# Performance work log

Hardware: AMD Instinct MI355X
Metric: run time of the kernel (lower is better)

## Reference

```python
import jax, jax.numpy as jnp
import numpy as np


def _conv3d(x, w, pad, groups=1):
    # x: [N,C,D,H,W]; w: [O,I/groups,kd,kh,kw]; cross-correlation, same as torch conv3d
    return jax.lax.conv_general_dilated(
        x, w, window_strides=(1, 1, 1),
        padding=[(p, p) for p in pad],
        dimension_numbers=('NCDHW', 'OIDHW', 'NCDHW'),
        feature_group_count=groups)


def setup_inputs() -> dict:
    key = jax.random.key(0)
    D = 192
    x = jax.random.normal(key, (1, 1, D, D, D), dtype=jnp.float32)

    # Gaussian kernel: sigma=1.0 -> radius=3 -> 7^3
    sigma = 1.0
    radius = int(3 * sigma)
    c = jnp.arange(-radius, radius + 1, dtype=jnp.float32)
    g1 = jnp.exp(-c ** 2 / (2.0 * sigma * sigma))
    g1 = g1 / g1.sum()
    g3 = g1[:, None, None] * g1[None, :, None] * g1[None, None, :]
    gauss3d = g3[None, None]  # [1,1,7,7,7]

    # Pavel derivative kernels (outer products of d [len 9] and s [len 5])
    d = jnp.array([2.0, 1.0, -16.0, -27.0, 0.0, 27.0, 16.0, -1.0, -2.0], dtype=jnp.float32)
    s = jnp.array([1.0, 4.0, 6.0, 4.0, 1.0], dtype=jnp.float32)
    norm = 96.0 * 16.0 * 16.0
    kz = (d[:, None, None] * s[None, :, None] * s[None, None, :] / norm)[None, None]  # [1,1,9,5,5]
    ky = (s[:, None, None] * d[None, :, None] * s[None, None, :] / norm)[None, None]  # [1,1,5,9,5]
    kx = (s[:, None, None] * s[None, :, None] * d[None, None, :] / norm)[None, None]  # [1,1,5,5,9]

    return {"x": x, "gauss3d": gauss3d, "kz": kz, "ky": ky, "kx": kx}


def reference(x, gauss3d, kz, ky, kx):
    pad = (gauss3d.shape[2] - 1) // 2  # radius = 3
    # sigma > 0: pre-smooth input
    xs = _conv3d(x, gauss3d, (pad, pad, pad))
    # gradient components
    gz = _conv3d(xs, kz, (4, 2, 2))
    gy = _conv3d(xs, ky, (2, 4, 2))
    gx = _conv3d(xs, kx, (2, 2, 4))
    # structure-tensor components, channel order [Jzz, Jzy, Jzx, Jyy, Jyx, Jxx]
    J = jnp.concatenate([gz * gz, gy * gz, gx * gz, gy * gy, gx * gy, gx * gx], axis=1)
    # smooth_components=True: grouped Gaussian smoothing of each component
    g6 = jnp.broadcast_to(gauss3d, (6,) + gauss3d.shape[1:])  # [6,1,7,7,7]
    J = _conv3d(J, g6, (pad, pad, pad), groups=6)
    return J
```

## Files before the change

### kernel.cpp

```cpp
#include <hip/hip_runtime.h>


constexpr int D  = 192;
constexpr int DD = D * D;
constexpr long long V = (long long)D * DD;

__global__ void setup_coef(const float* __restrict__ g3, const float* __restrict__ kz,
                           const float* __restrict__ ky, const float* __restrict__ kx,
                           float* __restrict__ c) {
    if (blockIdx.x != 0 || threadIdx.x != 0) return;
    float Tg = g3[0];
    for (int i = 0; i < 7; ++i) c[0 + i]  = g3[i * 49];
    for (int j = 0; j < 7; ++j) c[7 + j]  = g3[j * 7] / Tg;
    for (int k = 0; k < 7; ++k) c[14 + k] = g3[k] / Tg;
    float Tz = kz[0];
    for (int i = 0; i < 9; ++i) c[21 + i] = kz[i * 25];
    for (int j = 0; j < 5; ++j) c[30 + j] = kz[j * 5] / Tz;
    for (int k = 0; k < 5; ++k) c[35 + k] = kz[k] / Tz;
    float Ty = ky[0];
    for (int i = 0; i < 5; ++i) c[40 + i] = ky[i * 45];
    for (int j = 0; j < 9; ++j) c[45 + j] = ky[j * 5] / Ty;
    for (int k = 0; k < 5; ++k) c[54 + k] = ky[k] / Ty;
    float Tx = kx[0];
    for (int i = 0; i < 5; ++i) c[59 + i] = kx[i * 45];
    for (int j = 0; j < 5; ++j) c[64 + j] = kx[j * 9] / Tx;
    for (int k = 0; k < 9; ++k) c[69 + k] = kx[k] / Tx;
}

__device__ inline float4 ldg4(const float* __restrict__ slice, int gy, int gx) {
    float4 v = {0.f, 0.f, 0.f, 0.f};
    if ((unsigned)gy < (unsigned)D) {
        const float* row = slice + gy * D;
        if ((unsigned)gx <= (unsigned)(D - 4)) {
            v = *(const float4*)(row + gx);
        } else {
            float* pv = (float*)&v;
#pragma unroll
            for (int j = 0; j < 4; ++j) {
                const int g = gx + j;
                if ((unsigned)g < (unsigned)D) pv[j] = row[g];
            }
        }
    }
    return v;
}

__device__ inline void ldg4x2(const float* __restrict__ slA, const float* __restrict__ slB,
                              int gy, int gx, float4& a, float4& b) {
    a = make_float4(0.f, 0.f, 0.f, 0.f);
    b = a;
    if ((unsigned)gy < (unsigned)D) {
        const int ro = gy * D;
        if ((unsigned)gx <= (unsigned)(D - 4)) {
            a = *(const float4*)(slA + ro + gx);
            b = *(const float4*)(slB + ro + gx);
        } else {
            float* pa = (float*)&a;
            float* pb = (float*)&b;
#pragma unroll
            for (int j = 0; j < 4; ++j) {
                const int g = gx + j;
                if ((unsigned)g < (unsigned)D) { pa[j] = slA[ro + g]; pb[j] = slB[ro + g]; }
            }
        }
    }
}

__device__ inline float4 ld_task10(const float* __restrict__ slice, int y0, int x0, int li) {
    const int r = li / 10, q = li % 10;
    return ldg4(slice, y0 + r, x0 + q * 4);
}
__device__ inline void st_task41(float* __restrict__ dst, int li, float4 v) {
    const int r = li / 10, q = li % 10;
    float* d = &dst[r * 41 + q * 4];
    d[0] = v.x; d[1] = v.y; d[2] = v.z; d[3] = v.w;
}

template <int SEG>
__global__ __launch_bounds__(256) void blur3d_s1(const float* __restrict__ in,
                                                 float* __restrict__ out,
                                                 const float* __restrict__ coef) {
    __shared__ float raw[22 * 41];
    __shared__ float xt[22][32];
    const int cpx = gridDim.x >> 3;
    int w = (blockIdx.x & 7) * cpx + (blockIdx.x >> 3);
    const int tile = w % 72;
    const int seg = w / 72;
    const int tx0 = (tile % 6) * 32, ty0 = (tile / 6) * 16;
    const int z0 = seg * SEG;
    float ga[7], gb[7], gc[7];
#pragma unroll
    for (int k = 0; k < 7; ++k) { ga[k] = coef[k]; gb[k] = coef[7 + k]; gc[k] = coef[14 + k]; }
    const int tid = threadIdx.x;
    const int rr = tid >> 4;
    const int cc = (tid & 15) * 2;
    float2 ring[7];
#pragma unroll
    for (int k = 0; k < 7; ++k) ring[k] = make_float2(0.f, 0.f);

    for (int s = z0 - 3; s < z0 + SEG + 3; ++s) {
        const bool inz = (s >= 0 && s < D);
        if (inz && tid < 220) {
            const float* sl = in + (long long)s * DD;
            st_task41(raw, tid, ld_task10(sl, ty0 - 3, tx0 - 4, tid));
        }
        __syncthreads();
        if (inz && tid < 176) {
            const int r = tid >> 3, g = tid & 7;
            const float* rp = &raw[r * 41 + 4 * g + 1];
            float win[10];
#pragma unroll
            for (int i = 0; i < 10; ++i) win[i] = rp[i];
            float4 o = make_float4(0.f, 0.f, 0.f, 0.f);
#pragma unroll
            for (int k = 0; k < 7; ++k) {
                o.x += gc[k] * win[k];
                o.y += gc[k] * win[k + 1];
                o.z += gc[k] * win[k + 2];
                o.w += gc[k] * win[k + 3];
            }
            *(float4*)&xt[r][4 * g] = o;
        }
        __syncthreads();
        float2 yv = make_float2(0.f, 0.f);
        if (inz) {
#pragma unroll
            for (int k = 0; k < 7; ++k) {
                const float2 v = *(const float2*)&xt[rr + k][cc];
                yv.x += gb[k] * v.x; yv.y += gb[k] * v.y;
            }
        }
#pragma unroll
        for (int k = 0; k < 6; ++k) ring[k] = ring[k + 1];
        ring[6] = yv;
        const int z = s - 3;
        if (z >= z0) {
            float2 a = make_float2(0.f, 0.f);
#pragma unroll
            for (int k = 0; k < 7; ++k) {
                a.x += ga[k] * ring[k].x; a.y += ga[k] * ring[k].y;
            }
            *(float2*)(out + (long long)z * DD + (ty0 + rr) * D + tx0 + cc) = a;
        }
    }
}

template <int SEG, int NCH, bool PROD>
__global__ __launch_bounds__(256) void blur3d(const float* __restrict__ in,
                                              float* __restrict__ out,
                                              const float* __restrict__ coef) {
    __shared__ float raw[38 * 41];
    __shared__ float xt[38][32];
    const int cpx = gridDim.x >> 3;
    int w = (blockIdx.x & 7) * cpx + (blockIdx.x >> 3);
    const int tile = w % 36; w /= 36;
    const int ch = w % NCH;
    const int seg = w / NCH;
    const int tx0 = (tile % 6) * 32, ty0 = (tile / 6) * 32;
    const int z0 = seg * SEG;
    const int IA[6] = {0, 1, 2, 1, 2, 2};
    const int IB[6] = {0, 0, 0, 1, 1, 2};
    const float* srcA = in + (long long)(PROD ? IA[ch] : ch) * V;
    const float* srcB = in + (long long)(PROD ? IB[ch] : ch) * V;
    const bool same = !PROD || (IA[ch] == IB[ch]);
    float* dst = out + (long long)ch * V;
    float ga[7], gb[7], gc[7];
#pragma unroll
    for (int k = 0; k < 7; ++k) { ga[k] = coef[k]; gb[k] = coef[7 + k]; gc[k] = coef[14 + k]; }
    const int rr = threadIdx.x >> 3;
    const int cc = (threadIdx.x & 7) * 4;
    float4 ring[7];
#pragma unroll
    for (int k = 0; k < 7; ++k) ring[k] = make_float4(0.f, 0.f, 0.f, 0.f);

    for (int s = z0 - 3; s < z0 + SEG + 3; ++s) {
        const bool inz = (s >= 0 && s < D);
        if (inz) {
            const float* slA = srcA + (long long)s * DD;
            const float* slB = srcB + (long long)s * DD;
            if (same) {
                for (int li = threadIdx.x; li < 380; li += 256) {
                    float4 a = ld_task10(slA, ty0 - 3, tx0 - 4, li);
                    if (PROD) { a.x *= a.x; a.y *= a.y; a.z *= a.z; a.w *= a.w; }
                    st_task41(raw, li, a);
                }
            } else {
                for (int li = threadIdx.x; li < 380; li += 256) {
                    const int r = li / 10, q = li % 10;
                    float4 a, b;
                    ldg4x2(slA, slB, ty0 - 3 + r, tx0 - 4 + q * 4, a, b);
                    a.x *= b.x; a.y *= b.y; a.z *= b.z; a.w *= b.w;
                    float* d = &raw[r * 41 + q * 4];
                    d[0] = a.x; d[1] = a.y; d[2] = a.z; d[3] = a.w;
                }
            }
        }
        __syncthreads();
        if (inz) {
            for (int li = threadIdx.x; li < 38 * 8; li += 256) {
                const int r = li >> 3, g = li & 7;
                const float* rp = &raw[r * 41 + 4 * g + 1];
                float win[10];
#pragma unroll
                for (int i = 0; i < 10; ++i) win[i] = rp[i];
                float4 o = make_float4(0.f, 0.f, 0.f, 0.f);
#pragma unroll
                for (int k = 0; k < 7; ++k) {
                    o.x += gc[k] * win[k];
                    o.y += gc[k] * win[k + 1];
                    o.z += gc[k] * win[k + 2];
                    o.w += gc[k] * win[k + 3];
                }
                *(float4*)&xt[r][4 * g] = o;
            }
        }
        __syncthreads();
        float4 yv = make_float4(0.f, 0.f, 0.f, 0.f);
        if (inz) {
#pragma unroll
            for (int k = 0; k < 7; ++k) {
                const float4 v = *(const float4*)&xt[rr + k][cc];
                yv.x += gb[k] * v.x; yv.y += gb[k] * v.y;
                yv.z += gb[k] * v.z; yv.w += gb[k] * v.w;
            }
        }
#pragma unroll
        for (int k = 0; k < 6; ++k) ring[k] = ring[k + 1];
        ring[6] = yv;
        const int z = s - 3;
        if (z >= z0) {
            float4 a = make_float4(0.f, 0.f, 0.f, 0.f);
#pragma unroll
            for (int k = 0; k < 7; ++k) {
                a.x += ga[k] * ring[k].x; a.y += ga[k] * ring[k].y;
                a.z += ga[k] * ring[k].z; a.w += ga[k] * ring[k].w;
            }
            *(float4*)(dst + (long long)z * DD + (ty0 + rr) * D + tx0 + cc) = a;
        }
    }
}

template <int SEG>
__global__ __launch_bounds__(256) void grad3d(const float* __restrict__ xs,
                                              float* __restrict__ G,
                                              const float* __restrict__ coef) {
    __shared__ float raw[24 * 41];
    __shared__ float X1[24][32];
    __shared__ float X2[24][32];
    const int cpx = gridDim.x >> 3;
    int w = (blockIdx.x & 7) * cpx + (blockIdx.x >> 3);
    const int tile = w % 72;
    const int seg = w / 72;
    const int tx0 = (tile % 6) * 32, ty0 = (tile / 6) * 16;
    const int z0 = seg * SEG;
    float az[9], ay[5], ax[5], bz[5], by[9], bx[5], czc[5], cxc[9];
#pragma unroll
    for (int k = 0; k < 9; ++k) az[k] = coef[21 + k];
#pragma unroll
    for (int k = 0; k < 5; ++k) ay[k] = coef[40 + k];
#pragma unroll
    for (int k = 0; k < 5; ++k) ax[k] = coef[59 + k];
#pragma unroll
    for (int k = 0; k < 5; ++k) bz[k] = coef[30 + k];
#pragma unroll
    for (int k = 0; k < 9; ++k) by[k] = coef[45 + k];
#pragma unroll
    for (int k = 0; k < 5; ++k) bx[k] = coef[64 + k];
#pragma unroll
    for (int k = 0; k < 5; ++k) czc[k] = coef[35 + k];
#pragma unroll
    for (int k = 0; k < 9; ++k) cxc[k] = coef[69 + k];
    const int rr = threadIdx.x >> 4;
    const int cc = (threadIdx.x & 15) * 2;
    float2 R1[9], R2[7], R3[7];
#pragma unroll
    for (int k = 0; k < 9; ++k) R1[k] = make_float2(0.f, 0.f);
#pragma unroll
    for (int k = 0; k < 7; ++k) { R2[k] = make_float2(0.f, 0.f); R3[k] = make_float2(0.f, 0.f); }

    for (int s = z0 - 4; s < z0 + SEG + 4; ++s) {
        const bool inz = (s >= 0 && s < D);
        if (inz) {
            const float* sl = xs + (long long)s * DD;
            for (int li = threadIdx.x; li < 240; li += 256)
                st_task41(raw, li, ld_task10(sl, ty0 - 4, tx0 - 4, li));
        }
        __syncthreads();
        if (inz && threadIdx.x < 192) {
            const int r = threadIdx.x >> 3, g = threadIdx.x & 7;
            const float* rp = &raw[r * 41 + 4 * g];
            float win[12];
#pragma unroll
            for (int i = 0; i < 12; ++i) win[i] = rp[i];
            float4 o1 = make_float4(0.f, 0.f, 0.f, 0.f);
            float4 o2 = make_float4(0.f, 0.f, 0.f, 0.f);
#pragma unroll
            for (int k = 0; k < 5; ++k) {
                o1.x += czc[k] * win[2 + k];
                o1.y += czc[k] * win[3 + k];
                o1.z += czc[k] * win[4 + k];
                o1.w += czc[k] * win[5 + k];
            }
#pragma unroll
            for (int k = 0; k < 9; ++k) {
                o2.x += cxc[k] * win[k];
                o2.y += cxc[k] * win[1 + k];
                o2.z += cxc[k] * win[2 + k];
                o2.w += cxc[k] * win[3 + k];
            }
            *(float4*)&X1[r][4 * g] = o1;
            *(float4*)&X2[r][4 * g] = o2;
        }
        __syncthreads();
        float2 t1 = make_float2(0.f, 0.f), t2 = t1, t3 = t1;
        if (inz) {
#pragma unroll
            for (int k = 0; k < 5; ++k) {
                const float2 v = *(const float2*)&X1[rr + 2 + k][cc];
                t1.x += bz[k] * v.x; t1.y += bz[k] * v.y;
            }
#pragma unroll
            for (int k = 0; k < 9; ++k) {
                const float2 v = *(const float2*)&X1[rr + k][cc];
                t2.x += by[k] * v.x; t2.y += by[k] * v.y;
            }
#pragma unroll
            for (int k = 0; k < 5; ++k) {
                const float2 v = *(const float2*)&X2[rr + 2 + k][cc];
                t3.x += bx[k] * v.x; t3.y += bx[k] * v.y;
            }
        }
#pragma unroll
        for (int k = 0; k < 8; ++k) R1[k] = R1[k + 1];
        R1[8] = t1;
#pragma unroll
        for (int k = 0; k < 6; ++k) { R2[k] = R2[k + 1]; R3[k] = R3[k + 1]; }
        R2[6] = t2; R3[6] = t3;
        const int z = s - 4;
        if (z >= z0) {
            float gz0 = 0.f, gz1 = 0.f, gy0 = 0.f, gy1 = 0.f, gx0 = 0.f, gx1 = 0.f;
#pragma unroll
            for (int k = 0; k < 9; ++k) { gz0 += az[k] * R1[k].x; gz1 += az[k] * R1[k].y; }
#pragma unroll
            for (int k = 0; k < 5; ++k) {
                gy0 += ay[k] * R2[k].x; gy1 += ay[k] * R2[k].y;
                gx0 += ax[k] * R3[k].x; gx1 += ax[k] * R3[k].y;
            }
            float* o = G + (long long)z * DD + (ty0 + rr) * D + tx0 + cc;
            float2 wv;
            wv.x = gz0; wv.y = gz1; *(float2*)(o + 0 * V) = wv;
            wv.x = gy0; wv.y = gy1; *(float2*)(o + 1 * V) = wv;
            wv.x = gx0; wv.y = gx1; *(float2*)(o + 2 * V) = wv;
        }
    }
}

extern "C" void kernel_launch(void* const* d_in, const int* in_sizes, int n_in,
                              void* d_out, int out_size, void* d_ws, size_t ws_size,
                              hipStream_t stream) {
    const float* x  = (const float*)d_in[0];
    const float* g3 = (const float*)d_in[1];
    const float* kz = (const float*)d_in[2];
    const float* ky = (const float*)d_in[3];
    const float* kx = (const float*)d_in[4];
    float* out = (float*)d_out;

    float* coef = (float*)d_ws;
    float* G  = coef + 128;
    float* xs = G + 3 * V;

    setup_coef<<<1, 64, 0, stream>>>(g3, kz, ky, kx, coef);

    blur3d_s1<12><<<1152, 256, 0, stream>>>(x, xs, coef);

    grad3d<16><<<864, 256, 0, stream>>>(xs, G, coef);

    blur3d<32, 6, true><<<1296, 256, 0, stream>>>(G, out, coef);
}
```

Before: 164.9 us.

## Group structure-tensor products into two blocks of three channels per tile

Replaces the per-channel product-and-blur kernel with a grouped kernel in which each block loads the gradient slices once and forms three products (Jzz,Jzy,Jzx or Jyy,Jyx,Jxx), blurring all three together. This cuts redundant global reads of the gradient fields, which were previously reloaded for every output channel. Tiles change to 32x16 with a z-segment of 24, so shared memory and register use go up (three ring buffers, three xt tiles), which may lower occupancy.

```diff
diff --git a/kernel.cpp b/kernel.cpp
--- a/kernel.cpp
+++ b/kernel.cpp
@@ -45,27 +45,6 @@
     return v;
 }
 
-__device__ inline void ldg4x2(const float* __restrict__ slA, const float* __restrict__ slB,
-                              int gy, int gx, float4& a, float4& b) {
-    a = make_float4(0.f, 0.f, 0.f, 0.f);
-    b = a;
-    if ((unsigned)gy < (unsigned)D) {
-        const int ro = gy * D;
-        if ((unsigned)gx <= (unsigned)(D - 4)) {
-            a = *(const float4*)(slA + ro + gx);
-            b = *(const float4*)(slB + ro + gx);
-        } else {
-            float* pa = (float*)&a;
-            float* pb = (float*)&b;
-#pragma unroll
-            for (int j = 0; j < 4; ++j) {
-                const int g = gx + j;
-                if ((unsigned)g < (unsigned)D) { pa[j] = slA[ro + g]; pb[j] = slB[ro + g]; }
-            }
-        }
-    }
-}
-
 __device__ inline float4 ld_task10(const float* __restrict__ slice, int y0, int x0, int li) {
     const int r = li / 10, q = li % 10;
     return ldg4(slice, y0 + r, x0 + q * 4);
@@ -145,97 +124,117 @@
     }
 }
 
-template <int SEG, int NCH, bool PROD>
-__global__ __launch_bounds__(256) void blur3d(const float* __restrict__ in,
-                                              float* __restrict__ out,
-                                              const float* __restrict__ coef) {
-    __shared__ float raw[38 * 41];
-    __shared__ float xt[38][32];
+template <int SEG>
+__global__ __launch_bounds__(256) void blur3d_grp(const float* __restrict__ G,
+                                                  float* __restrict__ out,
+                                                  const float* __restrict__ coef) {
+    __shared__ float raw[3][22 * 41];
+    __shared__ float xt[3][22][32];
     const int cpx = gridDim.x >> 3;
     int w = (blockIdx.x & 7) * cpx + (blockIdx.x >> 3);
-    const int tile = w % 36; w /= 36;
-    const int ch = w % NCH;
-    const int seg = w / NCH;
-    const int tx0 = (tile % 6) * 32, ty0 = (tile / 6) * 32;
+    const int tile = w % 72; w /= 72;
+    const int grp = w & 1;
+    const int seg = w >> 1;
+    const int tx0 = (tile % 6) * 32, ty0 = (tile / 6) * 16;
     const int z0 = seg * SEG;
-    const int IA[6] = {0, 1, 2, 1, 2, 2};
-    const int IB[6] = {0, 0, 0, 1, 1, 2};
-    const float* srcA = in + (long long)(PROD ? IA[ch] : ch) * V;
-    const float* srcB = in + (long long)(PROD ? IB[ch] : ch) * V;
-    const bool same = !PROD || (IA[ch] == IB[ch]);
-    float* dst = out + (long long)ch * V;
+    const int nf = grp ? 2 : 3;
+    const float* F0 = G + (long long)(grp ? 1 : 0) * V;
+    const float* F1 = G + (long long)(grp ? 2 : 1) * V;
+    const float* F2 = G + 2 * V;
+    float* dst = out + (long long)(grp * 3) * V;
     float ga[7], gb[7], gc[7];
 #pragma unroll
     for (int k = 0; k < 7; ++k) { ga[k] = coef[k]; gb[k] = coef[7 + k]; gc[k] = coef[14 + k]; }
-    const int rr = threadIdx.x >> 3;
-    const int cc = (threadIdx.x & 7) * 4;
-    float4 ring[7];
-#pragma unroll
-    for (int k = 0; k < 7; ++k) ring[k] = make_float4(0.f, 0.f, 0.f, 0.f);
+    const int tid = threadIdx.x;
+    const int rr = tid >> 4;
+    const int cc = (tid & 15) * 2;
+    float2 R0[7], R1[7], R2[7];
+#pragma unroll
+    for (int k = 0; k < 7; ++k) {
+        R0[k] = make_float2(0.f, 0.f);
+        R1[k] = make_float2(0.f, 0.f);
+        R2[k] = make_float2(0.f, 0.f);
+    }
 
     for (int s = z0 - 3; s < z0 + SEG + 3; ++s) {
         const bool inz = (s >= 0 && s < D);
         if (inz) {
-            const float* slA = srcA + (long long)s * DD;
-            const float* slB = srcB + (long long)s * DD;
-            if (same) {
-                for (int li = threadIdx.x; li < 380; li += 256) {
-                    float4 a = ld_task10(slA, ty0 - 3, tx0 - 4, li);
-                    if (PROD) { a.x *= a.x; a.y *= a.y; a.z *= a.z; a.w *= a.w; }
-                    st_task41(raw, li, a);
+            const long long so = (long long)s * DD;
+            for (int li = tid; li < nf * 220; li += 256) {
+                const int f = li / 220, t = li - f * 220;
+                const float* sl = (f == 0 ? F0 : (f == 1 ? F1 : F2)) + so;
+                st_task41(raw[f], t, ld_task10(sl, ty0 - 3, tx0 - 4, t));
+            }
+        }
+        __syncthreads();
+        if (inz && tid < 176) {
+            const int r = tid >> 3, g = tid & 7;
+            const int off = r * 41 + 4 * g + 1;
+            float wA[10], wB[10];
+#pragma unroll
+            for (int i = 0; i < 10; ++i) { wA[i] = raw[0][off + i]; wB[i] = raw[1][off + i]; }
+            float p0[10], p1[10], p2[10];
+            if (grp == 0) {
+                float wC[10];
+#pragma unroll
+                for (int i = 0; i < 10; ++i) wC[i] = raw[2][off + i];
+#pragma unroll
+                for (int i = 0; i < 10; ++i) {
+                    p0[i] = wA[i] * wA[i];
+                    p1[i] = wB[i] * wA[i];
+                    p2[i] = wC[i] * wA[i];
                 }
             } else {
-                for (int li = threadIdx.x; li < 380; li += 256) {
-                    const int r = li / 10, q = li % 10;
-                    float4 a, b;
-                    ldg4x2(slA, slB, ty0 - 3 + r, tx0 - 4 + q * 4, a, b);
-                    a.x *= b.x; a.y *= b.y; a.z *= b.z; a.w *= b.w;
-                    float* d = &raw[r * 41 + q * 4];
-                    d[0] = a.x; d[1] = a.y; d[2] = a.z; d[3] = a.w;
+#pragma unroll
+                for (int i = 0; i < 10; ++i) {
+                    p0[i] = wA[i] * wA[i];
+                    p1[i] = wB[i] * wA[i];
+                    p2[i] = wB[i] * wB[i];
                 }
             }
-        }
-        __syncthreads();
-        if (inz) {
-            for (int li = threadIdx.x; li < 38 * 8; li += 256) {
-                const int r = li >> 3, g = li & 7;
-                const float* rp = &raw[r * 41 + 4 * g + 1];
-                float win[10];
-#pragma unroll
-                for (int i = 0; i < 10; ++i) win[i] = rp[i];
-                float4 o = make_float4(0.f, 0.f, 0.f, 0.f);
-#pragma unroll
-                for (int k = 0; k < 7; ++k) {
-                    o.x += gc[k] * win[k];
-                    o.y += gc[k] * win[k + 1];
-                    o.z += gc[k] * win[k + 2];
-                    o.w += gc[k] * win[k + 3];
-                }
-                *(float4*)&xt[r][4 * g] = o;
-            }
-        }
-        __syncthreads();
-        float4 yv = make_float4(0.f, 0.f, 0.f, 0.f);
-        if (inz) {
-#pragma unroll
-            for (int k = 0; k < 7; ++k) {
-                const float4 v = *(const float4*)&xt[rr + k][cc];
-                yv.x += gb[k] * v.x; yv.y += gb[k] * v.y;
-                yv.z += gb[k] * v.z; yv.w += gb[k] * v.w;
-            }
-        }
-#pragma unroll
-        for (int k = 0; k < 6; ++k) ring[k] = ring[k + 1];
-        ring[6] = yv;
+            float4 o0 = make_float4(0.f, 0.f, 0.f, 0.f), o1 = o0, o2 = o0;
+#pragma unroll
+            for (int k = 0; k < 7; ++k) {
+                o0.x += gc[k] * p0[k];     o0.y += gc[k] * p0[k + 1];
+                o0.z += gc[k] * p0[k + 2]; o0.w += gc[k] * p0[k + 3];
+                o1.x += gc[k] * p1[k];     o1.y += gc[k] * p1[k + 1];
+                o1.z += gc[k] * p1[k + 2]; o1.w += gc[k] * p1[k + 3];
+                o2.x += gc[k] * p2[k];     o2.y += gc[k] * p2[k + 1];
+                o2.z += gc[k] * p2[k + 2]; o2.w += gc[k] * p2[k + 3];
+            }
+            *(float4*)&xt[0][r][4 * g] = o0;
+            *(float4*)&xt[1][r][4 * g] = o1;
+            *(float4*)&xt[2][r][4 * g] = o2;
+        }
+        __syncthreads();
+        float2 y0 = make_float2(0.f, 0.f), y1 = y0, y2 = y0;
+        if (inz) {
+#pragma unroll
+            for (int k = 0; k < 7; ++k) {
+                const float2 v0 = *(const float2*)&xt[0][rr + k][cc];
+                const float2 v1 = *(const float2*)&xt[1][rr + k][cc];
+                const float2 v2 = *(const float2*)&xt[2][rr + k][cc];
+                y0.x += gb[k] * v0.x; y0.y += gb[k] * v0.y;
+                y1.x += gb[k] * v1.x; y1.y += gb[k] * v1.y;
+                y2.x += gb[k] * v2.x; y2.y += gb[k] * v2.y;
+            }
+        }
+#pragma unroll
+        for (int k = 0; k < 6; ++k) { R0[k] = R0[k + 1]; R1[k] = R1[k + 1]; R2[k] = R2[k + 1]; }
+        R0[6] = y0; R1[6] = y1; R2[6] = y2;
         const int z = s - 3;
         if (z >= z0) {
-            float4 a = make_float4(0.f, 0.f, 0.f, 0.f);
-#pragma unroll
-            for (int k = 0; k < 7; ++k) {
-                a.x += ga[k] * ring[k].x; a.y += ga[k] * ring[k].y;
-                a.z += ga[k] * ring[k].z; a.w += ga[k] * ring[k].w;
-            }
-            *(float4*)(dst + (long long)z * DD + (ty0 + rr) * D + tx0 + cc) = a;
+            float2 a0 = make_float2(0.f, 0.f), a1 = a0, a2 = a0;
+#pragma unroll
+            for (int k = 0; k < 7; ++k) {
+                a0.x += ga[k] * R0[k].x; a0.y += ga[k] * R0[k].y;
+                a1.x += ga[k] * R1[k].x; a1.y += ga[k] * R1[k].y;
+                a2.x += ga[k] * R2[k].x; a2.y += ga[k] * R2[k].y;
+            }
+            float* o = dst + (long long)z * DD + (ty0 + rr) * D + tx0 + cc;
+            *(float2*)(o + 0 * V) = a0;
+            *(float2*)(o + 1 * V) = a1;
+            *(float2*)(o + 2 * V) = a2;
         }
     }
 }
@@ -375,5 +374,5 @@
 
     grad3d<16><<<864, 256, 0, stream>>>(xs, G, coef);
 
-    blur3d<32, 6, true><<<1296, 256, 0, stream>>>(G, out, coef);
-}
+    blur3d_grp<24><<<1152, 256, 0, stream>>>(G, out, coef);
+}
```

Measured after the change: 205.8 us. 24.8% more time.

## Double-buffer shared staging in final blur to overlap loads and drop a barrier

Applied to the files above, without the earlier changes.

The six-channel product blur kernel now keeps two shared raw/xt buffers. It prefetches the next z-slice's product tile while computing the current slice's x-pass, which removes one __syncthreads per slice. This is meant to hide global load latency behind compute and reduce barrier stalls. In exchange, shared memory per block doubles, which could lower occupancy.

```diff
diff --git a/kernel.cpp b/kernel.cpp
--- a/kernel.cpp
+++ b/kernel.cpp
@@ -76,6 +76,27 @@
     d[0] = v.x; d[1] = v.y; d[2] = v.z; d[3] = v.w;
 }
 
+template <bool PROD>
+__device__ inline void stage_s3(const float* __restrict__ slA, const float* __restrict__ slB,
+                                bool same, float* __restrict__ dst, int ty0, int tx0) {
+    if (same) {
+        for (int li = threadIdx.x; li < 380; li += 256) {
+            float4 a = ld_task10(slA, ty0 - 3, tx0 - 4, li);
+            if (PROD) { a.x *= a.x; a.y *= a.y; a.z *= a.z; a.w *= a.w; }
+            st_task41(dst, li, a);
+        }
+    } else {
+        for (int li = threadIdx.x; li < 380; li += 256) {
+            const int r = li / 10, q = li % 10;
+            float4 a, b;
+            ldg4x2(slA, slB, ty0 - 3 + r, tx0 - 4 + q * 4, a, b);
+            a.x *= b.x; a.y *= b.y; a.z *= b.z; a.w *= b.w;
+            float* d = &dst[r * 41 + q * 4];
+            d[0] = a.x; d[1] = a.y; d[2] = a.z; d[3] = a.w;
+        }
+    }
+}
+
 template <int SEG>
 __global__ __launch_bounds__(256) void blur3d_s1(const float* __restrict__ in,
                                                  float* __restrict__ out,
@@ -146,11 +167,11 @@
 }
 
 template <int SEG, int NCH, bool PROD>
-__global__ __launch_bounds__(256) void blur3d(const float* __restrict__ in,
-                                              float* __restrict__ out,
-                                              const float* __restrict__ coef) {
-    __shared__ float raw[38 * 41];
-    __shared__ float xt[38][32];
+__global__ __launch_bounds__(256) void blur3d_db(const float* __restrict__ in,
+                                                 float* __restrict__ out,
+                                                 const float* __restrict__ coef) {
+    __shared__ float raw[2][38 * 41];
+    __shared__ float xt[2][38][32];
     const int cpx = gridDim.x >> 3;
     int w = (blockIdx.x & 7) * cpx + (blockIdx.x >> 3);
     const int tile = w % 36; w /= 36;
@@ -167,39 +188,28 @@
     float ga[7], gb[7], gc[7];
 #pragma unroll
     for (int k = 0; k < 7; ++k) { ga[k] = coef[k]; gb[k] = coef[7 + k]; gc[k] = coef[14 + k]; }
-    const int rr = threadIdx.x >> 3;
-    const int cc = (threadIdx.x & 7) * 4;
+    const int tid = threadIdx.x;
+    const int rr = tid >> 3;
+    const int cc = (tid & 7) * 4;
     float4 ring[7];
 #pragma unroll
     for (int k = 0; k < 7; ++k) ring[k] = make_float4(0.f, 0.f, 0.f, 0.f);
 
+    {
+        const int s0 = z0 - 3;
+        if (s0 >= 0 && s0 < D)
+            stage_s3<PROD>(srcA + (long long)s0 * DD, srcB + (long long)s0 * DD,
+                           same, raw[0], ty0, tx0);
+    }
+    __syncthreads();
+
+    int cur = 0;
     for (int s = z0 - 3; s < z0 + SEG + 3; ++s) {
         const bool inz = (s >= 0 && s < D);
         if (inz) {
-            const float* slA = srcA + (long long)s * DD;
-            const float* slB = srcB + (long long)s * DD;
-            if (same) {
-                for (int li = threadIdx.x; li < 380; li += 256) {
-                    float4 a = ld_task10(slA, ty0 - 3, tx0 - 4, li);
-                    if (PROD) { a.x *= a.x; a.y *= a.y; a.z *= a.z; a.w *= a.w; }
-                    st_task41(raw, li, a);
-                }
-            } else {
-                for (int li = threadIdx.x; li < 380; li += 256) {
-                    const int r = li / 10, q = li % 10;
-                    float4 a, b;
-                    ldg4x2(slA, slB, ty0 - 3 + r, tx0 - 4 + q * 4, a, b);
-                    a.x *= b.x; a.y *= b.y; a.z *= b.z; a.w *= b.w;
-                    float* d = &raw[r * 41 + q * 4];
-                    d[0] = a.x; d[1] = a.y; d[2] = a.z; d[3] = a.w;
-                }
-            }
-        }
-        __syncthreads();
-        if (inz) {
-            for (int li = threadIdx.x; li < 38 * 8; li += 256) {
+            for (int li = tid; li < 38 * 8; li += 256) {
                 const int r = li >> 3, g = li & 7;
-                const float* rp = &raw[r * 41 + 4 * g + 1];
+                const float* rp = &raw[cur][r * 41 + 4 * g + 1];
                 float win[10];
 #pragma unroll
                 for (int i = 0; i < 10; ++i) win[i] = rp[i];
@@ -211,15 +221,19 @@
                     o.z += gc[k] * win[k + 2];
                     o.w += gc[k] * win[k + 3];
                 }
-                *(float4*)&xt[r][4 * g] = o;
-            }
-        }
+                *(float4*)&xt[cur][r][4 * g] = o;
+            }
+        }
+        const int sn = s + 1;
+        if (sn < z0 + SEG + 3 && sn >= 0 && sn < D)
+            stage_s3<PROD>(srcA + (long long)sn * DD, srcB + (long long)sn * DD,
+                           same, raw[cur ^ 1], ty0, tx0);
         __syncthreads();
         float4 yv = make_float4(0.f, 0.f, 0.f, 0.f);
         if (inz) {
 #pragma unroll
             for (int k = 0; k < 7; ++k) {
-                const float4 v = *(const float4*)&xt[rr + k][cc];
+                const float4 v = *(const float4*)&xt[cur][rr + k][cc];
                 yv.x += gb[k] * v.x; yv.y += gb[k] * v.y;
                 yv.z += gb[k] * v.z; yv.w += gb[k] * v.w;
             }
@@ -237,6 +251,7 @@
             }
             *(float4*)(dst + (long long)z * DD + (ty0 + rr) * D + tx0 + cc) = a;
         }
+        cur ^= 1;
     }
 }
 
@@ -375,5 +390,5 @@
 
     grad3d<16><<<864, 256, 0, stream>>>(xs, G, coef);
 
-    blur3d<32, 6, true><<<1296, 256, 0, stream>>>(G, out, coef);
-}
+    blur3d_db<32, 6, true><<<1296, 256, 0, stream>>>(G, out, coef);
+}
```

Result: no change. 162.9 us (-1.2%).
